# Performance work log

Hardware: AMD Instinct MI355X
Metric: run time of the kernel (lower is better)

Reference implementation:

```python
import jax, jax.numpy as jnp
import numpy as np
import math

B = 2
H = 16
M = 1024
D = 64      # head_dim
P = 1024    # persistent memory size
SPAN = 1024 # external attention span


def setup_inputs() -> dict:
    key = jax.random.key(0)
    k1, k2, k3, k4 = jax.random.split(key, 4)
    query = jax.random.normal(k1, (B * H, M, D), dtype=jnp.float32)
    attn = jax.random.normal(k2, (B * H, M, SPAN), dtype=jnp.float32)
    # params as in __init__
    pkey = jax.random.normal(k3, (H, D, P), dtype=jnp.float32) / math.sqrt(D)
    pval = jax.random.normal(k4, (H, P, D), dtype=jnp.float32) / math.sqrt(P)
    return {"query": query, "attn": attn, "key": pkey, "val": pval}


def reference(query, attn, key, val):
    h, d, p = key.shape
    bh, m, _ = query.shape
    q = query.reshape(-1, h, m, d)                      # [B,H,M,D]
    # attn_pers = q @ (key * sqrt(d)); later divided by sqrt(d) -> net q@key
    attn_pers = jnp.einsum('bhmd,hdp->bhmp', q, key * math.sqrt(d))
    attn_pers = attn_pers.reshape(-1, m, p)             # [B*H,M,P]
    scores = jnp.concatenate([attn, attn_pers], axis=-1) / math.sqrt(d)
    probs = jax.nn.softmax(scores, axis=-1)             # [B*H,M,SPAN+P]
    attn_out = probs[:, :, :-p]                         # [B*H,M,SPAN]
    pers = probs[:, :, -p:].reshape(-1, h, m, p)        # [B,H,M,P]
    out = jnp.einsum('bhmp,hpd->bhmd', pers, val * math.sqrt(p))
    out = out.reshape(-1, m, d)                         # [B*H,M,D]
    return (attn_out, out)
```

## Files before the change

### kernel.cpp

```cpp
#include <hip/hip_runtime.h>
#include <hip/hip_bf16.h>
#include <math.h>

#define BH   32
#define NH   16
#define MM   1024
#define DD   64
#define PP   1024
#define SPAN 1024

typedef unsigned short ushort_t;
typedef __attribute__((ext_vector_type(8))) short  short8;
typedef __attribute__((ext_vector_type(4))) float  f32x4;

#define MFMA(a,b,c) __builtin_amdgcn_mfma_f32_16x16x32_bf16(a,b,c,0,0,0)

#if __has_builtin(__builtin_amdgcn_exp2f)
#define EXP2(x) __builtin_amdgcn_exp2f(x)
#else
#define EXP2(x) __expf((x) * 0.6931471805599453f)
#endif

#define ATTN_SC 0.18033688011111603f
#define LOG2E   1.4426950408889634f

#define WS_SA_OFF (4194304ull)
#define WS_SP_OFF (4325376ull)
#define WS_NEED   (4456448ull)

__device__ __forceinline__ ushort_t f2bf(float x) {
    __hip_bfloat16 b = __float2bfloat16(x);
    return __builtin_bit_cast(unsigned short, b);
}
__device__ __forceinline__ float bf2f(ushort_t u) {
    __hip_bfloat16 b = __builtin_bit_cast(__hip_bfloat16, u);
    return __bfloat162float(b);
}

__launch_bounds__(256)
__global__ void pm_pre(const float* __restrict__ key,
                       const float* __restrict__ val,
                       ushort_t* __restrict__ wsKV)
{
    int bi = blockIdx.x, t = threadIdx.x;
    if (bi < 512) {
        int id = bi * 256 + t;
        int l  = id & 63;
        int ks = (id >> 6) & 1;
        int pb = (id >> 7) & 3;
        int c  = (id >> 9) & 15;
        int h  = (id >> 13) & 15;
        int p     = c * 64 + pb * 16 + (l & 15);
        int dbase = ks * 32 + (l >> 4) * 8;
        size_t fo = (size_t)(h * 16 + c) * 8192 + (size_t)(pb * 2 + ks) * 512 + (size_t)l * 8;
#pragma unroll
        for (int e = 0; e < 8; ++e)
            wsKV[fo + e] = f2bf(key[(size_t)(h * 64 + dbase + e) * PP + p] * LOG2E);
    } else {
        int id = (bi - 512) * 256 + t;
        int l   = id & 63;
        int db  = (id >> 6) & 3;
        int ks2 = (id >> 8) & 1;
        int c   = (id >> 9) & 15;
        int h   = (id >> 13) & 15;
        int d = db * 16 + (l & 15);
        size_t fo = (size_t)(h * 16 + c) * 8192 + 4096 + (size_t)(ks2 * 4 + db) * 512 + (size_t)l * 8;
#pragma unroll
        for (int e = 0; e < 8; ++e) {
            int p = c * 64 + ks2 * 32 + ((l >> 4) * 4) + (e & 3) + 16 * (e >> 2);
            wsKV[fo + e] = f2bf(val[(size_t)(h * PP + p) * DD + d]);
        }
    }
}

__launch_bounds__(256)
__global__ void pm_work(const float* __restrict__ q,
                        const float* __restrict__ attn,
                        const ushort_t* __restrict__ wsKV,
                        float* __restrict__ ws_sa,
                        float* __restrict__ ws_sp,
                        float* __restrict__ out)
{
    __shared__ ushort_t kvbuf[2][8192];

    const int t  = threadIdx.x;
    const int w  = t >> 6;
    const int l  = t & 63;
    const int bi = blockIdx.x;
    const int hi = l >> 4;
    const int lo = l & 15;

    if ((bi & 1) == 0) {
        const int fi   = bi >> 1;
        const int bh   = fi & 31;
        const int tile = fi >> 5;
        const int h    = bh & (NH - 1);
        const size_t rowbase = (size_t)bh * MM + tile * 64;

        short8 qf[2][2];
        {
            const float* qr = q + (rowbase + w * 16 + lo) * DD + hi * 8;
#pragma unroll
            for (int ks = 0; ks < 2; ++ks) {
                float4 a = *(const float4*)(qr + ks * 32);
                float4 b = *(const float4*)(qr + ks * 32 + 4);
                float f[8] = {a.x, a.y, a.z, a.w, b.x, b.y, b.z, b.w};
                short8 qh, ql;
#pragma unroll
                for (int e = 0; e < 8; ++e) {
                    ushort_t hh = f2bf(f[e]);
                    qh[e] = (short)hh;
                    ql[e] = (short)f2bf(f[e] - bf2f(hh));
                }
                qf[ks][0] = qh;
                qf[ks][1] = ql;
            }
        }

        const ushort_t* KVb = wsKV + (size_t)h * (16 * 8192);

        auto STAGE = [&](int b, int c) {
            const char* src = (const char*)(KVb + (size_t)c * 8192) + w * 4096 + l * 16;
            char* dst = (char*)&kvbuf[b][0] + w * 4096;
#pragma unroll
            for (int j = 0; j < 4; ++j)
                __builtin_amdgcn_global_load_lds(
                    (const __attribute__((address_space(1))) void*)(src + j * 1024),
                    (__attribute__((address_space(3))) void*)(dst + j * 1024),
                    16, 0, 0);
        };

        f32x4 oacc[4] = {{0.f,0.f,0.f,0.f},{0.f,0.f,0.f,0.f},{0.f,0.f,0.f,0.f},{0.f,0.f,0.f,0.f}};
        float spart = 0.f;

        STAGE(0, 0);
        __syncthreads();

        for (int c = 0; c < 16; ++c) {
            const int cur = c & 1;
            if (c < 15) STAGE(cur ^ 1, c + 1);

            const ushort_t* Kc = &kvbuf[cur][0];
            const ushort_t* Vc = Kc + 4096;

            f32x4 sacc[4] = {{0.f,0.f,0.f,0.f},{0.f,0.f,0.f,0.f},{0.f,0.f,0.f,0.f},{0.f,0.f,0.f,0.f}};
            __builtin_amdgcn_s_setprio(1);
#pragma unroll
            for (int pb = 0; pb < 4; ++pb) {
#pragma unroll
                for (int ks = 0; ks < 2; ++ks) {
                    short8 khi = *(const short8*)(Kc + (pb * 2 + ks) * 512 + l * 8);
                    sacc[pb] = MFMA(khi, qf[ks][0], sacc[pb]);
                    sacc[pb] = MFMA(khi, qf[ks][1], sacc[pb]);
                }
            }
            __builtin_amdgcn_s_setprio(0);

            float ep[4][4];
#pragma unroll
            for (int pb = 0; pb < 4; ++pb)
#pragma unroll
                for (int r = 0; r < 4; ++r) {
                    float pv = EXP2(sacc[pb][r]);
                    ep[pb][r] = pv;
                    spart += pv;
                }

            short8 pf[2][2];
#pragma unroll
            for (int ks2 = 0; ks2 < 2; ++ks2) {
                short8 phi8, plo8;
#pragma unroll
                for (int e = 0; e < 8; ++e) {
                    float pv = ep[ks2 * 2 + (e >> 2)][e & 3];
                    ushort_t hh = f2bf(pv);
                    phi8[e] = (short)hh;
                    plo8[e] = (short)f2bf(pv - bf2f(hh));
                }
                pf[ks2][0] = phi8;
                pf[ks2][1] = plo8;
            }

            __builtin_amdgcn_s_setprio(1);
#pragma unroll
            for (int ks2 = 0; ks2 < 2; ++ks2) {
#pragma unroll
                for (int db = 0; db < 4; ++db) {
                    short8 vhi = *(const short8*)(Vc + (ks2 * 4 + db) * 512 + l * 8);
                    oacc[db] = MFMA(pf[ks2][0], vhi, oacc[db]);
                    oacc[db] = MFMA(pf[ks2][1], vhi, oacc[db]);
                }
            }
            __builtin_amdgcn_s_setprio(0);

            __syncthreads();
        }

        spart += __shfl_xor(spart, 16);
        spart += __shfl_xor(spart, 32);
        if (hi == 0) ws_sp[rowbase + w * 16 + lo] = spart;

#pragma unroll
        for (int reg = 0; reg < 4; ++reg) {
            const size_t ro = (rowbase + w * 16 + hi * 4 + reg) * DD + lo;
#pragma unroll
            for (int db = 0; db < 4; ++db)
                __builtin_nontemporal_store(oacc[db][reg], &out[ro + db * 16]);
        }
    } else {
        const int si   = bi >> 1;
        const int bh   = si & 31;
        const int tile = si >> 5;
        const size_t rowbase = (size_t)bh * MM + tile * 64;

        for (int rp = 0; rp < 8; ++rp) {
            const int r0 = w * 16 + rp * 2;
            const f32x4* a0 = (const f32x4*)(attn + (rowbase + r0) * SPAN);
            const f32x4* a1 = (const f32x4*)(attn + (rowbase + r0 + 1) * SPAN);
            f32x4 v0[4], v1[4];
#pragma unroll
            for (int j = 0; j < 4; ++j) v0[j] = a0[j * 64 + l];
#pragma unroll
            for (int j = 0; j < 4; ++j) v1[j] = a1[j * 64 + l];

            float s0 = 0.f, s1 = 0.f;
#pragma unroll
            for (int j = 0; j < 4; ++j)
#pragma unroll
                for (int e = 0; e < 4; ++e) {
                    s0 += EXP2(v0[j][e] * ATTN_SC);
                    s1 += EXP2(v1[j][e] * ATTN_SC);
                }
#pragma unroll
            for (int s = 1; s < 64; s <<= 1) {
                s0 += __shfl_xor(s0, s);
                s1 += __shfl_xor(s1, s);
            }
            if (l == 0) {
                ws_sa[rowbase + r0]     = s0;
                ws_sa[rowbase + r0 + 1] = s1;
            }
        }
    }
}

__launch_bounds__(256)
__global__ void pm_norm(const float* __restrict__ attn,
                        const float* __restrict__ ws_sa,
                        const float* __restrict__ ws_sp,
                        float* __restrict__ attn_out,
                        float* __restrict__ out)
{
    const int t = threadIdx.x;
    const int w = t >> 6;
    const int l = t & 63;
    const size_t row = (size_t)blockIdx.x * 4 + w;

    const float iZ = 1.f / (ws_sa[row] + ws_sp[row]);

    const f32x4* arow = (const f32x4*)(attn + row * SPAN);
    f32x4 av[4];
#pragma unroll
    for (int j = 0; j < 4; ++j) av[j] = arow[j * 64 + l];
    const float ov = out[row * DD + l];

    f32x4* orow = (f32x4*)(attn_out + row * SPAN);
#pragma unroll
    for (int j = 0; j < 4; ++j) {
        f32x4 o;
#pragma unroll
        for (int e = 0; e < 4; ++e) o[e] = EXP2(av[j][e] * ATTN_SC) * iZ;
        __builtin_nontemporal_store(o, orow + j * 64 + l);
    }
    __builtin_nontemporal_store(ov * 32.f * iZ, &out[row * DD + l]);
}

__launch_bounds__(256)
__global__ void pm_fallback(const float* __restrict__ q,
                            const float* __restrict__ attn,
                            const float* __restrict__ key,
                            const float* __restrict__ val,
                            float* __restrict__ attn_out,
                            float* __restrict__ out)
{
    __shared__ float qs[64][68];
    __shared__ float ks[64][68];
    __shared__ float vs[64][DD];
    __shared__ float sc[64][66];
    __shared__ float rmax[64];
    __shared__ float rsum[64];

    const int t    = threadIdx.x;
    const int bh   = blockIdx.y;
    const int tile = blockIdx.x;
    const int h    = bh & (NH - 1);
    const int m0   = tile * 64;
    const int tr   = t >> 4;
    const int tc   = t & 15;
    const int r0   = tr * 4;
    const int c0   = tc * 4;
    const int lane = t & 63;
    const int wave = t >> 6;

    const size_t qbase = (size_t)bh * MM * DD + (size_t)m0 * DD;
    const size_t abase = (size_t)bh * MM * SPAN + (size_t)m0 * SPAN;
    const size_t kbase = (size_t)h * DD * PP;
    const size_t vbase = (size_t)h * PP * DD;

#pragma unroll
    for (int j = 0; j < 16; ++j) {
        int idx = j * 256 + t;
        int r = idx >> 6, d = idx & 63;
        qs[r][d] = q[qbase + (size_t)r * DD + d];
    }
    for (int rr = 0; rr < 16; ++rr) {
        int r = wave * 16 + rr;
        const float* arow = attn + abase + (size_t)r * SPAN;
        float av[16];
        float mx = -INFINITY;
#pragma unroll
        for (int j = 0; j < 16; ++j) { av[j] = arow[j * 64 + lane] * 0.125f; mx = fmaxf(mx, av[j]); }
#pragma unroll
        for (int s = 32; s; s >>= 1) mx = fmaxf(mx, __shfl_xor(mx, s));
        float sm = 0.f;
#pragma unroll
        for (int j = 0; j < 16; ++j) sm += __expf(av[j] - mx);
#pragma unroll
        for (int s = 32; s; s >>= 1) sm += __shfl_xor(sm, s);
        if (lane == 0) { rmax[r] = mx; rsum[r] = sm; }
    }
    __syncthreads();
    for (int p0 = 0; p0 < PP; p0 += 64) {
        if (p0) __syncthreads();
#pragma unroll
        for (int j = 0; j < 16; ++j) {
            int idx = j * 256 + t;
            int d = idx >> 6, pc = idx & 63;
            ks[pc][d] = key[kbase + (size_t)d * PP + p0 + pc];
        }
        __syncthreads();
        float acc[4][4] = {};
#pragma unroll
        for (int d0 = 0; d0 < DD; d0 += 4) {
            float4 q4[4], k4[4];
#pragma unroll
            for (int rr = 0; rr < 4; ++rr) q4[rr] = *(const float4*)&qs[r0 + rr][d0];
#pragma unroll
            for (int cc = 0; cc < 4; ++cc) k4[cc] = *(const float4*)&ks[c0 + cc][d0];
#pragma unroll
            for (int rr = 0; rr < 4; ++rr)
#pragma unroll
                for (int cc = 0; cc < 4; ++cc)
                    acc[rr][cc] += q4[rr].x * k4[cc].x + q4[rr].y * k4[cc].y
                                 + q4[rr].z * k4[cc].z + q4[rr].w * k4[cc].w;
        }
#pragma unroll
        for (int rr = 0; rr < 4; ++rr) {
            float mx = fmaxf(fmaxf(acc[rr][0], acc[rr][1]), fmaxf(acc[rr][2], acc[rr][3]));
#pragma unroll
            for (int s = 8; s; s >>= 1) mx = fmaxf(mx, __shfl_xor(mx, s));
            float sm = 0.f;
#pragma unroll
            for (int cc = 0; cc < 4; ++cc) sm += __expf(acc[rr][cc] - mx);
#pragma unroll
            for (int s = 8; s; s >>= 1) sm += __shfl_xor(sm, s);
            if (tc == 0) {
                int r = r0 + rr;
                float om = rmax[r], os = rsum[r];
                float nm = fmaxf(om, mx);
                rsum[r] = os * __expf(om - nm) + sm * __expf(mx - nm);
                rmax[r] = nm;
            }
        }
    }
    __syncthreads();
    for (int rr = 0; rr < 16; ++rr) {
        int r = wave * 16 + rr;
        float Mx = rmax[r];
        float iZ = 1.0f / rsum[r];
        const float* arow = attn + abase + (size_t)r * SPAN;
        float* orow = attn_out + abase + (size_t)r * SPAN;
#pragma unroll
        for (int j = 0; j < 16; ++j) {
            float a = arow[j * 64 + lane] * 0.125f;
            orow[j * 64 + lane] = __expf(a - Mx) * iZ;
        }
    }
    float acc2[4][4] = {};
    for (int p0 = 0; p0 < PP; p0 += 64) {
        __syncthreads();
#pragma unroll
        for (int j = 0; j < 16; ++j) {
            int idx = j * 256 + t;
            int d = idx >> 6, pc = idx & 63;
            ks[pc][d] = key[kbase + (size_t)d * PP + p0 + pc];
        }
#pragma unroll
        for (int j = 0; j < 16; ++j) {
            int idx = j * 256 + t;
            int pc = idx >> 6, d = idx & 63;
            vs[pc][d] = val[vbase + (size_t)(p0 + pc) * DD + d];
        }
        __syncthreads();
        float acc[4][4] = {};
#pragma unroll
        for (int d0 = 0; d0 < DD; d0 += 4) {
            float4 q4[4], k4[4];
#pragma unroll
            for (int rr = 0; rr < 4; ++rr) q4[rr] = *(const float4*)&qs[r0 + rr][d0];
#pragma unroll
            for (int cc = 0; cc < 4; ++cc) k4[cc] = *(const float4*)&ks[c0 + cc][d0];
#pragma unroll
            for (int rr = 0; rr < 4; ++rr)
#pragma unroll
                for (int cc = 0; cc < 4; ++cc)
                    acc[rr][cc] += q4[rr].x * k4[cc].x + q4[rr].y * k4[cc].y
                                 + q4[rr].z * k4[cc].z + q4[rr].w * k4[cc].w;
        }
#pragma unroll
        for (int rr = 0; rr < 4; ++rr) {
            float Mx = rmax[r0 + rr];
#pragma unroll
            for (int cc = 0; cc < 4; ++cc)
                sc[r0 + rr][c0 + cc] = __expf(acc[rr][cc] - Mx);
        }
        __syncthreads();
        for (int pc = 0; pc < 64; ++pc) {
            float4 v4 = *(const float4*)&vs[pc][tc * 4];
#pragma unroll
            for (int rr = 0; rr < 4; ++rr) {
                float pr = sc[r0 + rr][pc];
                acc2[rr][0] += pr * v4.x;
                acc2[rr][1] += pr * v4.y;
                acc2[rr][2] += pr * v4.z;
                acc2[rr][3] += pr * v4.w;
            }
        }
    }
#pragma unroll
    for (int rr = 0; rr < 4; ++rr) {
        int r = r0 + rr;
        float s = 32.0f / rsum[r];
        float4 o;
        o.x = acc2[rr][0] * s; o.y = acc2[rr][1] * s;
        o.z = acc2[rr][2] * s; o.w = acc2[rr][3] * s;
        *(float4*)&out[(size_t)bh * MM * DD + (size_t)(m0 + r) * DD + tc * 4] = o;
    }
}

extern "C" void kernel_launch(void* const* d_in, const int* in_sizes, int n_in,
                              void* d_out, int out_size, void* d_ws, size_t ws_size,
                              hipStream_t stream) {
    const float* q    = (const float*)d_in[0];
    const float* attn = (const float*)d_in[1];
    const float* key  = (const float*)d_in[2];
    const float* val  = (const float*)d_in[3];
    float* attn_out = (float*)d_out;
    float* out      = (float*)d_out + (size_t)BH * MM * SPAN;

    if (ws_size >= WS_NEED) {
        ushort_t* wsKV  = (ushort_t*)d_ws;
        float*    ws_sa = (float*)((char*)d_ws + WS_SA_OFF);
        float*    ws_sp = (float*)((char*)d_ws + WS_SP_OFF);
        pm_pre <<<1024, 256, 0, stream>>>(key, val, wsKV);
        pm_work<<<1024, 256, 0, stream>>>(q, attn, wsKV, ws_sa, ws_sp, out);
        pm_norm<<<8192, 256, 0, stream>>>(attn, ws_sa, ws_sp, attn_out, out);
    } else {
        dim3 grid(MM / 64, BH);
        pm_fallback<<<grid, 256, 0, stream>>>(q, attn, key, val, attn_out, out);
    }
}
```

Measured before the change: 87.83 us.

## Split persistent-memory attention over P into two halves across blocks

Each 64-row tile's pass over the persistent key/value dimension is split into two blocks, one per half of the 16 chunks. Each half writes its partial softmax sum and partial output to workspace, and the normalization kernel combines them. The aim is more parallelism (1536 blocks instead of 1024) and a shorter serial chunk loop per block. The cost is extra workspace traffic for a second output buffer and sum array, plus one more read per row in the norm pass.

```diff
diff --git a/kernel.cpp b/kernel.cpp
--- a/kernel.cpp
+++ b/kernel.cpp
@@ -24,9 +24,11 @@
 #define ATTN_SC 0.18033688011111603f
 #define LOG2E   1.4426950408889634f
 
-#define WS_SA_OFF (4194304ull)
-#define WS_SP_OFF (4325376ull)
-#define WS_NEED   (4456448ull)
+#define WS_SA_OFF  (4194304ull)
+#define WS_SP0_OFF (4325376ull)
+#define WS_SP1_OFF (4456448ull)
+#define WS_O1_OFF  (4587520ull)
+#define WS_NEED    (12976128ull)
 
 __device__ __forceinline__ ushort_t f2bf(float x) {
     __hip_bfloat16 b = __float2bfloat16(x);
@@ -78,7 +80,9 @@
                         const float* __restrict__ attn,
                         const ushort_t* __restrict__ wsKV,
                         float* __restrict__ ws_sa,
-                        float* __restrict__ ws_sp,
+                        float* __restrict__ ws_sp0,
+                        float* __restrict__ ws_sp1,
+                        float* __restrict__ o1,
                         float* __restrict__ out)
 {
     __shared__ ushort_t kvbuf[2][8192];
@@ -90,12 +94,15 @@
     const int hi = l >> 4;
     const int lo = l & 15;
 
-    if ((bi & 1) == 0) {
-        const int fi   = bi >> 1;
-        const int bh   = fi & 31;
-        const int tile = fi >> 5;
-        const int h    = bh & (NH - 1);
-        const size_t rowbase = (size_t)bh * MM + tile * 64;
+    const int ty   = bi % 3;
+    const int unit = bi / 3;
+    const int bh   = unit & 31;
+    const int tile = unit >> 5;
+    const size_t rowbase = (size_t)bh * MM + tile * 64;
+
+    if (ty < 2) {
+        const int s = ty;
+        const int h = bh & (NH - 1);
 
         short8 qf[2][2];
         {
@@ -133,12 +140,12 @@
         f32x4 oacc[4] = {{0.f,0.f,0.f,0.f},{0.f,0.f,0.f,0.f},{0.f,0.f,0.f,0.f},{0.f,0.f,0.f,0.f}};
         float spart = 0.f;
 
-        STAGE(0, 0);
+        STAGE(0, s * 8);
         __syncthreads();
 
-        for (int c = 0; c < 16; ++c) {
-            const int cur = c & 1;
-            if (c < 15) STAGE(cur ^ 1, c + 1);
+        for (int cc = 0; cc < 8; ++cc) {
+            const int cur = cc & 1;
+            if (cc < 7) STAGE(cur ^ 1, s * 8 + cc + 1);
 
             const ushort_t* Kc = &kvbuf[cur][0];
             const ushort_t* Vc = Kc + 4096;
@@ -198,21 +205,18 @@
 
         spart += __shfl_xor(spart, 16);
         spart += __shfl_xor(spart, 32);
-        if (hi == 0) ws_sp[rowbase + w * 16 + lo] = spart;
-
+        float* spdst = s ? ws_sp1 : ws_sp0;
+        if (hi == 0) spdst[rowbase + w * 16 + lo] = spart;
+
+        float* odst = s ? o1 : out;
 #pragma unroll
         for (int reg = 0; reg < 4; ++reg) {
             const size_t ro = (rowbase + w * 16 + hi * 4 + reg) * DD + lo;
 #pragma unroll
             for (int db = 0; db < 4; ++db)
-                __builtin_nontemporal_store(oacc[db][reg], &out[ro + db * 16]);
+                __builtin_nontemporal_store(oacc[db][reg], &odst[ro + db * 16]);
         }
     } else {
-        const int si   = bi >> 1;
-        const int bh   = si & 31;
-        const int tile = si >> 5;
-        const size_t rowbase = (size_t)bh * MM + tile * 64;
-
         for (int rp = 0; rp < 8; ++rp) {
             const int r0 = w * 16 + rp * 2;
             const f32x4* a0 = (const f32x4*)(attn + (rowbase + r0) * SPAN);
@@ -247,7 +251,9 @@
 __launch_bounds__(256)
 __global__ void pm_norm(const float* __restrict__ attn,
                         const float* __restrict__ ws_sa,
-                        const float* __restrict__ ws_sp,
+                        const float* __restrict__ ws_sp0,
+                        const float* __restrict__ ws_sp1,
+                        const float* __restrict__ o1,
                         float* __restrict__ attn_out,
                         float* __restrict__ out)
 {
@@ -256,13 +262,14 @@
     const int l = t & 63;
     const size_t row = (size_t)blockIdx.x * 4 + w;
 
-    const float iZ = 1.f / (ws_sa[row] + ws_sp[row]);
+    const float iZ = 1.f / (ws_sa[row] + ws_sp0[row] + ws_sp1[row]);
 
     const f32x4* arow = (const f32x4*)(attn + row * SPAN);
     f32x4 av[4];
 #pragma unroll
     for (int j = 0; j < 4; ++j) av[j] = arow[j * 64 + l];
-    const float ov = out[row * DD + l];
+    const float ov0 = out[row * DD + l];
+    const float ov1 = o1[row * DD + l];
 
     f32x4* orow = (f32x4*)(attn_out + row * SPAN);
 #pragma unroll
@@ -272,7 +279,7 @@
         for (int e = 0; e < 4; ++e) o[e] = EXP2(av[j][e] * ATTN_SC) * iZ;
         __builtin_nontemporal_store(o, orow + j * 64 + l);
     }
-    __builtin_nontemporal_store(ov * 32.f * iZ, &out[row * DD + l]);
+    __builtin_nontemporal_store((ov0 + ov1) * 32.f * iZ, &out[row * DD + l]);
 }
 
 __launch_bounds__(256)
@@ -459,12 +466,14 @@
     float* out      = (float*)d_out + (size_t)BH * MM * SPAN;
 
     if (ws_size >= WS_NEED) {
-        ushort_t* wsKV  = (ushort_t*)d_ws;
-        float*    ws_sa = (float*)((char*)d_ws + WS_SA_OFF);
-        float*    ws_sp = (float*)((char*)d_ws + WS_SP_OFF);
+        ushort_t* wsKV   = (ushort_t*)d_ws;
+        float*    ws_sa  = (float*)((char*)d_ws + WS_SA_OFF);
+        float*    ws_sp0 = (float*)((char*)d_ws + WS_SP0_OFF);
+        float*    ws_sp1 = (float*)((char*)d_ws + WS_SP1_OFF);
+        float*    o1     = (float*)((char*)d_ws + WS_O1_OFF);
         pm_pre <<<1024, 256, 0, stream>>>(key, val, wsKV);
-        pm_work<<<1024, 256, 0, stream>>>(q, attn, wsKV, ws_sa, ws_sp, out);
-        pm_norm<<<8192, 256, 0, stream>>>(attn, ws_sa, ws_sp, attn_out, out);
+        pm_work<<<1536, 256, 0, stream>>>(q, attn, wsKV, ws_sa, ws_sp0, ws_sp1, o1, out);
+        pm_norm<<<8192, 256, 0, stream>>>(attn, ws_sa, ws_sp0, ws_sp1, o1, attn_out, out);
     } else {
         dim3 grid(MM / 64, BH);
         pm_fallback<<<grid, 256, 0, stream>>>(q, attn, key, val, attn_out, out);
```

Result: no change. 87.85 us (+0.0%).

## Fuse normalization into work kernel with per-tile flag handoff between block roles

Applied to the files above, without the earlier changes.

Merges the separate normalization kernel into the main kernel. Attention-side blocks compute row sums, spin-wait on a per-tile release flag set by the matching persistent-memory block, then write normalized attn_out and rescale out directly. This removes one kernel launch and the round-trip of partial sums through global memory. The cost is a hipMemsetAsync for flags, spin-wait stalls, a second read of attn rows, and a deadlock risk if consumer blocks are resident while their producers are not scheduled.

```diff
diff --git a/kernel.cpp b/kernel.cpp
--- a/kernel.cpp
+++ b/kernel.cpp
@@ -24,9 +24,9 @@
 #define ATTN_SC 0.18033688011111603f
 #define LOG2E   1.4426950408889634f
 
-#define WS_SA_OFF (4194304ull)
-#define WS_SP_OFF (4325376ull)
-#define WS_NEED   (4456448ull)
+#define WS_SP_OFF   (4194304ull)
+#define WS_FLAG_OFF (4325376ull)
+#define WS_NEED     (4327424ull)
 
 __device__ __forceinline__ ushort_t f2bf(float x) {
     __hip_bfloat16 b = __float2bfloat16(x);
@@ -74,14 +74,17 @@
 }
 
 __launch_bounds__(256)
-__global__ void pm_work(const float* __restrict__ q,
+__global__ void pm_pipe(const float* __restrict__ q,
                         const float* __restrict__ attn,
                         const ushort_t* __restrict__ wsKV,
-                        float* __restrict__ ws_sa,
                         float* __restrict__ ws_sp,
+                        int*   __restrict__ flags,
+                        float* __restrict__ attn_out,
                         float* __restrict__ out)
 {
     __shared__ ushort_t kvbuf[2][8192];
+    __shared__ float sa[64];
+    __shared__ float iZ[64];
 
     const int t  = threadIdx.x;
     const int w  = t >> 6;
@@ -90,12 +93,14 @@
     const int hi = l >> 4;
     const int lo = l & 15;
 
-    if ((bi & 1) == 0) {
-        const int fi   = bi >> 1;
-        const int bh   = fi & 31;
-        const int tile = fi >> 5;
-        const int h    = bh & (NH - 1);
-        const size_t rowbase = (size_t)bh * MM + tile * 64;
+    const int role = (bi >> 3) & 1;
+    const int unit = ((bi >> 4) << 3) | (bi & 7);
+    const int bh   = unit & 31;
+    const int tile = unit >> 5;
+    const size_t rowbase = (size_t)bh * MM + tile * 64;
+
+    if (role == 0) {
+        const int h = bh & (NH - 1);
 
         short8 qf[2][2];
         {
@@ -198,81 +203,65 @@
 
         spart += __shfl_xor(spart, 16);
         spart += __shfl_xor(spart, 32);
-        if (hi == 0) ws_sp[rowbase + w * 16 + lo] = spart;
+        if (hi == 0) ws_sp[(size_t)unit * 64 + w * 16 + lo] = spart;
 
 #pragma unroll
         for (int reg = 0; reg < 4; ++reg) {
             const size_t ro = (rowbase + w * 16 + hi * 4 + reg) * DD + lo;
 #pragma unroll
             for (int db = 0; db < 4; ++db)
-                __builtin_nontemporal_store(oacc[db][reg], &out[ro + db * 16]);
-        }
+                out[ro + db * 16] = oacc[db][reg];
+        }
+
+        __threadfence();
+        __syncthreads();
+        if (t == 0)
+            __hip_atomic_store(&flags[unit], 1, __ATOMIC_RELEASE, __HIP_MEMORY_SCOPE_AGENT);
     } else {
-        const int si   = bi >> 1;
-        const int bh   = si & 31;
-        const int tile = si >> 5;
-        const size_t rowbase = (size_t)bh * MM + tile * 64;
-
-        for (int rp = 0; rp < 8; ++rp) {
-            const int r0 = w * 16 + rp * 2;
-            const f32x4* a0 = (const f32x4*)(attn + (rowbase + r0) * SPAN);
-            const f32x4* a1 = (const f32x4*)(attn + (rowbase + r0 + 1) * SPAN);
-            f32x4 v0[4], v1[4];
-#pragma unroll
-            for (int j = 0; j < 4; ++j) v0[j] = a0[j * 64 + l];
-#pragma unroll
-            for (int j = 0; j < 4; ++j) v1[j] = a1[j * 64 + l];
-
-            float s0 = 0.f, s1 = 0.f;
+        for (int rr = 0; rr < 16; ++rr) {
+            const int r = w * 16 + rr;
+            const f32x4* arow = (const f32x4*)(attn + (rowbase + r) * SPAN);
+            f32x4 av[4];
+#pragma unroll
+            for (int j = 0; j < 4; ++j) av[j] = arow[j * 64 + l];
+            float sm = 0.f;
 #pragma unroll
             for (int j = 0; j < 4; ++j)
 #pragma unroll
-                for (int e = 0; e < 4; ++e) {
-                    s0 += EXP2(v0[j][e] * ATTN_SC);
-                    s1 += EXP2(v1[j][e] * ATTN_SC);
-                }
-#pragma unroll
-            for (int s = 1; s < 64; s <<= 1) {
-                s0 += __shfl_xor(s0, s);
-                s1 += __shfl_xor(s1, s);
-            }
-            if (l == 0) {
-                ws_sa[rowbase + r0]     = s0;
-                ws_sa[rowbase + r0 + 1] = s1;
-            }
-        }
-    }
-}
-
-__launch_bounds__(256)
-__global__ void pm_norm(const float* __restrict__ attn,
-                        const float* __restrict__ ws_sa,
-                        const float* __restrict__ ws_sp,
-                        float* __restrict__ attn_out,
-                        float* __restrict__ out)
-{
-    const int t = threadIdx.x;
-    const int w = t >> 6;
-    const int l = t & 63;
-    const size_t row = (size_t)blockIdx.x * 4 + w;
-
-    const float iZ = 1.f / (ws_sa[row] + ws_sp[row]);
-
-    const f32x4* arow = (const f32x4*)(attn + row * SPAN);
-    f32x4 av[4];
-#pragma unroll
-    for (int j = 0; j < 4; ++j) av[j] = arow[j * 64 + l];
-    const float ov = out[row * DD + l];
-
-    f32x4* orow = (f32x4*)(attn_out + row * SPAN);
-#pragma unroll
-    for (int j = 0; j < 4; ++j) {
-        f32x4 o;
-#pragma unroll
-        for (int e = 0; e < 4; ++e) o[e] = EXP2(av[j][e] * ATTN_SC) * iZ;
-        __builtin_nontemporal_store(o, orow + j * 64 + l);
-    }
-    __builtin_nontemporal_store(ov * 32.f * iZ, &out[row * DD + l]);
+                for (int e = 0; e < 4; ++e) sm += EXP2(av[j][e] * ATTN_SC);
+#pragma unroll
+            for (int s = 1; s < 64; s <<= 1) sm += __shfl_xor(sm, s);
+            if (l == 0) sa[r] = sm;
+        }
+        __syncthreads();
+
+        if (t == 0) {
+            while (__hip_atomic_load(&flags[unit], __ATOMIC_ACQUIRE, __HIP_MEMORY_SCOPE_AGENT) == 0)
+                __builtin_amdgcn_s_sleep(16);
+        }
+        __syncthreads();
+
+        if (t < 64) iZ[t] = 1.f / (sa[t] + ws_sp[(size_t)unit * 64 + t]);
+        __syncthreads();
+
+        for (int rr = 0; rr < 16; ++rr) {
+            const int r = w * 16 + rr;
+            const size_t row = rowbase + r;
+            const float z = iZ[r];
+            const f32x4* arow = (const f32x4*)(attn + row * SPAN);
+            f32x4*       orow = (f32x4*)(attn_out + row * SPAN);
+#pragma unroll
+            for (int j = 0; j < 4; ++j) {
+                f32x4 a = arow[j * 64 + l];
+                f32x4 o;
+#pragma unroll
+                for (int e = 0; e < 4; ++e) o[e] = EXP2(a[e] * ATTN_SC) * z;
+                __builtin_nontemporal_store(o, orow + j * 64 + l);
+            }
+            const float ov = out[row * DD + l];
+            __builtin_nontemporal_store(ov * 32.f * z, &out[row * DD + l]);
+        }
+    }
 }
 
 __launch_bounds__(256)
@@ -377,13 +366,13 @@
     for (int rr = 0; rr < 16; ++rr) {
         int r = wave * 16 + rr;
         float Mx = rmax[r];
-        float iZ = 1.0f / rsum[r];
+        float iZv = 1.0f / rsum[r];
         const float* arow = attn + abase + (size_t)r * SPAN;
         float* orow = attn_out + abase + (size_t)r * SPAN;
 #pragma unroll
         for (int j = 0; j < 16; ++j) {
             float a = arow[j * 64 + lane] * 0.125f;
-            orow[j * 64 + lane] = __expf(a - Mx) * iZ;
+            orow[j * 64 + lane] = __expf(a - Mx) * iZv;
         }
     }
     float acc2[4][4] = {};
@@ -460,11 +449,11 @@
 
     if (ws_size >= WS_NEED) {
         ushort_t* wsKV  = (ushort_t*)d_ws;
-        float*    ws_sa = (float*)((char*)d_ws + WS_SA_OFF);
         float*    ws_sp = (float*)((char*)d_ws + WS_SP_OFF);
+        int*      flags = (int*)((char*)d_ws + WS_FLAG_OFF);
+        hipMemsetAsync(flags, 0, 512 * sizeof(int), stream);
         pm_pre <<<1024, 256, 0, stream>>>(key, val, wsKV);
-        pm_work<<<1024, 256, 0, stream>>>(q, attn, wsKV, ws_sa, ws_sp, out);
-        pm_norm<<<8192, 256, 0, stream>>>(attn, ws_sa, ws_sp, attn_out, out);
+        pm_pipe<<<1024, 256, 0, stream>>>(q, attn, wsKV, ws_sp, flags, attn_out, out);
     } else {
         dim3 grid(MM / 64, BH);
         pm_fallback<<<grid, 256, 0, stream>>>(q, attn, key, val, attn_out, out);
```

After: 183.6 us. 2.09x slower.
